# Optimization experiments

Measured on AMD Instinct MI355X. Metric: run time of the kernel, lower is better.

Reference implementation:

```python
import jax, jax.numpy as jnp
import numpy as np

G, NODES, H, E = 64, 511, 768, 4096
N = NODES + 1  # +1 graph token


def setup_inputs() -> dict:
    key = jax.random.key(0)
    ks = jax.random.split(key, 7)
    node_emb = jax.random.normal(ks[0], (4, H), dtype=jnp.float32) * 0.02
    node_emb = node_emb.at[0].set(0.0)  # padding_idx=0
    graph_emb = jax.random.normal(ks[1], (1, H), dtype=jnp.float32) * 0.02
    W_l = jax.random.normal(ks[2], (H, H), dtype=jnp.float32) / np.sqrt(H)
    b_l = jnp.zeros((H,), dtype=jnp.float32)
    W_r = jax.random.normal(ks[3], (H, H), dtype=jnp.float32) / np.sqrt(H)
    input_nodes = jax.random.randint(ks[4], (G, NODES), 0, 4, dtype=jnp.int64) if jax.config.jax_enable_x64 else jax.random.randint(ks[4], (G, NODES), 0, 4, dtype=jnp.int32)
    input_edges = jax.random.randint(ks[5], (G, 2, E), 0, N, dtype=jnp.int32)
    return {"input_nodes": input_nodes, "input_edges": input_edges,
            "node_emb": node_emb, "graph_emb": graph_emb,
            "W_l": W_l, "b_l": b_l, "W_r": W_r}


def _sage_conv(x, edges, W_l, b_l, W_r):
    # PyG SAGEConv (mean aggr): out = lin_l(mean_{j in N(i)} x_j) + lin_r(x_i)
    # x: [G, N, H]; edges: [G, 2, E] (row0 = src, row1 = dst)
    g, n, h = x.shape
    src, dst = edges[:, 0, :], edges[:, 1, :]                       # [G, E]
    offs = (jnp.arange(g, dtype=src.dtype) * n)[:, None]
    fs = (src + offs).reshape(-1)                                   # flat src ids
    fd = (dst + offs).reshape(-1)                                   # flat dst ids
    xf = x.reshape(g * n, h)
    msg = xf[fs]                                                    # gather [G*E, H]
    agg = jax.ops.segment_sum(msg, fd, num_segments=g * n)          # scatter-add
    deg = jax.ops.segment_sum(jnp.ones_like(fd, dtype=x.dtype), fd, num_segments=g * n)
    mean = agg / jnp.maximum(deg, 1.0)[:, None]
    out = mean @ W_l.T + b_l + xf @ W_r.T
    return out.reshape(g, n, h)


def reference(input_nodes, input_edges, node_emb, graph_emb, W_l, b_l, W_r):
    g = input_nodes.shape[0]
    node_feature = node_emb[input_nodes]                            # [G, NODES, H]
    graph_token = jnp.broadcast_to(graph_emb[None], (g, 1, node_emb.shape[1]))
    graph_node_feature = jnp.concatenate([graph_token, node_feature], axis=1)  # [G, N, H]
    graph_edge_feature = _sage_conv(graph_node_feature, input_edges, W_l, b_l, W_r)
    return (graph_node_feature, graph_edge_feature)
```

## Files before the change

kernel.cpp:

```cpp
#include <hip/hip_runtime.h>

#define G_     64
#define NODES_ 511
#define NN_    512
#define H_     768
#define E_     4096
#define NTYPE  5

typedef float f32x4 __attribute__((ext_vector_type(4)));

__global__ __launch_bounds__(512)
void prep_kernel(const int* __restrict__ edges,
                 const int* __restrict__ nodes,
                 const float* __restrict__ node_emb,
                 const float* __restrict__ graph_emb,
                 const float* __restrict__ W_l,
                 const float* __restrict__ b_l,
                 const float* __restrict__ W_r,
                 int* __restrict__ cnt,
                 float* __restrict__ P_l,
                 float* __restrict__ P_r)
{
    if (blockIdx.x < G_) {
        __shared__ int hist[NN_ * NTYPE];
        int g = blockIdx.x;
        int t = threadIdx.x;

        #pragma unroll
        for (int i = 0; i < NN_ * NTYPE / 512; ++i)
            hist[t + i * 512] = 0;
        __syncthreads();

        const int* eg = edges + (size_t)g * 2 * E_;
        const int* ng = nodes + (size_t)g * NODES_;
        #pragma unroll
        for (int i = 0; i < E_ / 512; ++i) {
            int e = t + i * 512;
            int src = eg[e];
            int dst = eg[E_ + e];
            int type = (src == 0) ? 0 : (ng[src - 1] + 1);
            atomicAdd(&hist[dst * NTYPE + type], 1);
        }
        __syncthreads();

        int* cg = cnt + (size_t)g * NN_ * NTYPE;
        #pragma unroll
        for (int i = 0; i < NN_ * NTYPE / 512; ++i)
            cg[t + i * 512] = hist[t + i * 512];
    } else {
        int wave = (blockIdx.x - G_) * 8 + (threadIdx.x >> 6);
        int lane = threadIdx.x & 63;
        int m = wave / (NTYPE * H_);
        int r = wave % (NTYPE * H_);
        int t = r / H_;
        int j = r % H_;
        const float* emb = (t == 0) ? graph_emb : (node_emb + (size_t)(t - 1) * H_);
        const float* W   = ((m == 0) ? W_l : W_r) + (size_t)j * H_;

        float a0, a1, a2;
        {
            int k0 = lane * 4;
            f32x4 w0 = *(const f32x4*)(W + k0);
            f32x4 e0 = *(const f32x4*)(emb + k0);
            f32x4 w1 = *(const f32x4*)(W + k0 + 256);
            f32x4 e1 = *(const f32x4*)(emb + k0 + 256);
            f32x4 w2 = *(const f32x4*)(W + k0 + 512);
            f32x4 e2 = *(const f32x4*)(emb + k0 + 512);
            a0 = w0.x * e0.x + w0.y * e0.y + w0.z * e0.z + w0.w * e0.w;
            a1 = w1.x * e1.x + w1.y * e1.y + w1.z * e1.z + w1.w * e1.w;
            a2 = w2.x * e2.x + w2.y * e2.y + w2.z * e2.z + w2.w * e2.w;
        }
        float acc = a0 + a1 + a2;
        #pragma unroll
        for (int off = 32; off; off >>= 1)
            acc += __shfl_xor(acc, off, 64);

        if (lane == 0) {
            if (m == 0) P_l[t * H_ + j] = acc;
            else        P_r[t * H_ + j] = acc + b_l[j];
        }
    }
}

__global__ __launch_bounds__(256)
void out_kernel(const int* __restrict__ nodes,
                const int* __restrict__ cnt,
                const float* __restrict__ node_emb,
                const float* __restrict__ graph_emb,
                const float* __restrict__ P_l,
                const float* __restrict__ P_r,
                float* __restrict__ gnf,
                float* __restrict__ gef)
{
    int wave = blockIdx.x * 4 + (threadIdx.x >> 6);
    int lane = threadIdx.x & 63;
    int k0   = lane * 4;

    f32x4 pl[NTYPE][3];
    #pragma unroll
    for (int t = 0; t < NTYPE; ++t) {
        #pragma unroll
        for (int c = 0; c < 3; ++c)
            pl[t][c] = *(const f32x4*)(P_l + (size_t)t * H_ + k0 + c * 256);
    }

    int row0 = wave * 4;
    #pragma unroll
    for (int i = 0; i < 4; ++i) {
        int row = row0 + i;
        int g = row >> 9;
        int n = row & (NN_ - 1);

        int ty = (n == 0) ? 0 : (nodes[g * NODES_ + n - 1] + 1);

        const int* c = cnt + (size_t)row * NTYPE;
        float c0 = (float)c[0], c1 = (float)c[1], c2 = (float)c[2],
              c3 = (float)c[3], c4 = (float)c[4];
        float inv = 1.0f / fmaxf(c0 + c1 + c2 + c3 + c4, 1.0f);
        float a0 = c0 * inv, a1 = c1 * inv, a2 = c2 * inv,
              a3 = c3 * inv, a4 = c4 * inv;

        const float* prr = P_r + (size_t)ty * H_;
        const float* er  = (ty == 0) ? graph_emb : (node_emb + (size_t)(ty - 1) * H_);
        size_t roff = (size_t)row * H_ + k0;

        #pragma unroll
        for (int ch = 0; ch < 3; ++ch) {
            f32x4 pr = *(const f32x4*)(prr + k0 + ch * 256);
            f32x4 ev = *(const f32x4*)(er  + k0 + ch * 256);
            f32x4 o  = a0 * pl[0][ch] + a1 * pl[1][ch] + a2 * pl[2][ch]
                     + a3 * pl[3][ch] + a4 * pl[4][ch] + pr;
            __builtin_nontemporal_store(ev, (f32x4*)(gnf + roff + ch * 256));
            __builtin_nontemporal_store(o,  (f32x4*)(gef + roff + ch * 256));
        }
    }
}

extern "C" void kernel_launch(void* const* d_in, const int* in_sizes, int n_in,
                              void* d_out, int out_size, void* d_ws, size_t ws_size,
                              hipStream_t stream)
{
    const int*   input_nodes = (const int*)d_in[0];
    const int*   input_edges = (const int*)d_in[1];
    const float* node_emb    = (const float*)d_in[2];
    const float* graph_emb   = (const float*)d_in[3];
    const float* W_l         = (const float*)d_in[4];
    const float* b_l         = (const float*)d_in[5];
    const float* W_r         = (const float*)d_in[6];

    float* gnf = (float*)d_out;
    float* gef = gnf + (size_t)G_ * NN_ * H_;

    int*   cnt = (int*)d_ws;
    size_t cnt_bytes = (size_t)G_ * NN_ * NTYPE * sizeof(int);
    float* P_l = (float*)((char*)d_ws + cnt_bytes);
    float* P_r = P_l + NTYPE * H_;

    prep_kernel<<<G_ + (2 * NTYPE * H_) / 8, 512, 0, stream>>>(
        input_edges, input_nodes, node_emb, graph_emb, W_l, b_l, W_r,
        cnt, P_l, P_r);

    out_kernel<<<(G_ * NN_) / 16, 256, 0, stream>>>(
        input_nodes, cnt, node_emb, graph_emb, P_l, P_r, gnf, gef);
}
```

Baseline: 228.9 us.

## Move gnf writes into prep kernel and precompute per-node mean coefficients

```diff
diff --git a/kernel.cpp b/kernel.cpp
--- a/kernel.cpp
+++ b/kernel.cpp
@@ -6,6 +6,9 @@
 #define H_     768
 #define E_     4096
 #define NTYPE  5
+
+#define PROJB_ 960
+#define GNFB_  2048
 
 typedef float f32x4 __attribute__((ext_vector_type(4)));
 
@@ -17,14 +20,15 @@
                  const float* __restrict__ W_l,
                  const float* __restrict__ b_l,
                  const float* __restrict__ W_r,
-                 int* __restrict__ cnt,
+                 float* __restrict__ params,
                  float* __restrict__ P_l,
-                 float* __restrict__ P_r)
+                 float* __restrict__ P_r,
+                 float* __restrict__ gnf)
 {
+    int t = threadIdx.x;
     if (blockIdx.x < G_) {
         __shared__ int hist[NN_ * NTYPE];
         int g = blockIdx.x;
-        int t = threadIdx.x;
 
         #pragma unroll
         for (int i = 0; i < NN_ * NTYPE / 512; ++i)
@@ -43,18 +47,29 @@
         }
         __syncthreads();
 
-        int* cg = cnt + (size_t)g * NN_ * NTYPE;
-        #pragma unroll
-        for (int i = 0; i < NN_ * NTYPE / 512; ++i)
-            cg[t + i * 512] = hist[t + i * 512];
-    } else {
-        int wave = (blockIdx.x - G_) * 8 + (threadIdx.x >> 6);
-        int lane = threadIdx.x & 63;
+        {
+            int n = t;
+            float c0 = (float)hist[n * NTYPE + 0];
+            float c1 = (float)hist[n * NTYPE + 1];
+            float c2 = (float)hist[n * NTYPE + 2];
+            float c3 = (float)hist[n * NTYPE + 3];
+            float c4 = (float)hist[n * NTYPE + 4];
+            float inv = 1.0f / fmaxf(c0 + c1 + c2 + c3 + c4, 1.0f);
+            int ty = (n == 0) ? 0 : (ng[n - 1] + 1);
+            f32x4 v0 = {c0 * inv, c1 * inv, c2 * inv, c3 * inv};
+            f32x4 v1 = {c4 * inv, __int_as_float(ty), 0.0f, 0.0f};
+            float* pp = params + ((size_t)g * NN_ + n) * 8;
+            *(f32x4*)pp       = v0;
+            *(f32x4*)(pp + 4) = v1;
+        }
+    } else if (blockIdx.x < G_ + PROJB_) {
+        int wave = (blockIdx.x - G_) * 8 + (t >> 6);
+        int lane = t & 63;
         int m = wave / (NTYPE * H_);
         int r = wave % (NTYPE * H_);
-        int t = r / H_;
+        int ty = r / H_;
         int j = r % H_;
-        const float* emb = (t == 0) ? graph_emb : (node_emb + (size_t)(t - 1) * H_);
+        const float* emb = (ty == 0) ? graph_emb : (node_emb + (size_t)(ty - 1) * H_);
         const float* W   = ((m == 0) ? W_l : W_r) + (size_t)j * H_;
 
         float a0, a1, a2;
@@ -76,20 +91,35 @@
             acc += __shfl_xor(acc, off, 64);
 
         if (lane == 0) {
-            if (m == 0) P_l[t * H_ + j] = acc;
-            else        P_r[t * H_ + j] = acc + b_l[j];
+            if (m == 0) P_l[ty * H_ + j] = acc;
+            else        P_r[ty * H_ + j] = acc + b_l[j];
+        }
+    } else {
+        int wv   = (blockIdx.x - (G_ + PROJB_)) * 8 + (t >> 6);
+        int lane = t & 63;
+        int k0   = lane * 4;
+        #pragma unroll
+        for (int i = 0; i < 2; ++i) {
+            int row = wv * 2 + i;
+            int g = row >> 9;
+            int n = row & (NN_ - 1);
+            int ty = (n == 0) ? 0 : (nodes[g * NODES_ + n - 1] + 1);
+            const float* er = (ty == 0) ? graph_emb
+                                        : (node_emb + (size_t)(ty - 1) * H_);
+            size_t roff = (size_t)row * H_ + k0;
+            #pragma unroll
+            for (int c = 0; c < 3; ++c) {
+                f32x4 ev = *(const f32x4*)(er + k0 + c * 256);
+                *(f32x4*)(gnf + roff + c * 256) = ev;
+            }
         }
     }
 }
 
 __global__ __launch_bounds__(256)
-void out_kernel(const int* __restrict__ nodes,
-                const int* __restrict__ cnt,
-                const float* __restrict__ node_emb,
-                const float* __restrict__ graph_emb,
+void gef_kernel(const float* __restrict__ params,
                 const float* __restrict__ P_l,
                 const float* __restrict__ P_r,
-                float* __restrict__ gnf,
                 float* __restrict__ gef)
 {
     int wave = blockIdx.x * 4 + (threadIdx.x >> 6);
@@ -98,40 +128,29 @@
 
     f32x4 pl[NTYPE][3];
     #pragma unroll
-    for (int t = 0; t < NTYPE; ++t) {
+    for (int tt = 0; tt < NTYPE; ++tt) {
         #pragma unroll
         for (int c = 0; c < 3; ++c)
-            pl[t][c] = *(const f32x4*)(P_l + (size_t)t * H_ + k0 + c * 256);
+            pl[tt][c] = *(const f32x4*)(P_l + (size_t)tt * H_ + k0 + c * 256);
     }
 
     int row0 = wave * 4;
     #pragma unroll
     for (int i = 0; i < 4; ++i) {
         int row = row0 + i;
-        int g = row >> 9;
-        int n = row & (NN_ - 1);
-
-        int ty = (n == 0) ? 0 : (nodes[g * NODES_ + n - 1] + 1);
-
-        const int* c = cnt + (size_t)row * NTYPE;
-        float c0 = (float)c[0], c1 = (float)c[1], c2 = (float)c[2],
-              c3 = (float)c[3], c4 = (float)c[4];
-        float inv = 1.0f / fmaxf(c0 + c1 + c2 + c3 + c4, 1.0f);
-        float a0 = c0 * inv, a1 = c1 * inv, a2 = c2 * inv,
-              a3 = c3 * inv, a4 = c4 * inv;
-
+        const float* pp = params + (size_t)row * 8;
+        f32x4 v0 = *(const f32x4*)pp;
+        f32x4 v1 = *(const f32x4*)(pp + 4);
+        int ty = __float_as_int(v1.y);
         const float* prr = P_r + (size_t)ty * H_;
-        const float* er  = (ty == 0) ? graph_emb : (node_emb + (size_t)(ty - 1) * H_);
         size_t roff = (size_t)row * H_ + k0;
 
         #pragma unroll
-        for (int ch = 0; ch < 3; ++ch) {
-            f32x4 pr = *(const f32x4*)(prr + k0 + ch * 256);
-            f32x4 ev = *(const f32x4*)(er  + k0 + ch * 256);
-            f32x4 o  = a0 * pl[0][ch] + a1 * pl[1][ch] + a2 * pl[2][ch]
-                     + a3 * pl[3][ch] + a4 * pl[4][ch] + pr;
-            __builtin_nontemporal_store(ev, (f32x4*)(gnf + roff + ch * 256));
-            __builtin_nontemporal_store(o,  (f32x4*)(gef + roff + ch * 256));
+        for (int c = 0; c < 3; ++c) {
+            f32x4 pr = *(const f32x4*)(prr + k0 + c * 256);
+            f32x4 o  = v0.x * pl[0][c] + v0.y * pl[1][c] + v0.z * pl[2][c]
+                     + v0.w * pl[3][c] + v1.x * pl[4][c] + pr;
+            *(f32x4*)(gef + roff + c * 256) = o;
         }
     }
 }
@@ -151,15 +170,14 @@
     float* gnf = (float*)d_out;
     float* gef = gnf + (size_t)G_ * NN_ * H_;
 
-    int*   cnt = (int*)d_ws;
-    size_t cnt_bytes = (size_t)G_ * NN_ * NTYPE * sizeof(int);
-    float* P_l = (float*)((char*)d_ws + cnt_bytes);
+    float* params = (float*)d_ws;
+    float* P_l = params + (size_t)G_ * NN_ * 8;
     float* P_r = P_l + NTYPE * H_;
 
-    prep_kernel<<<G_ + (2 * NTYPE * H_) / 8, 512, 0, stream>>>(
+    prep_kernel<<<G_ + PROJB_ + GNFB_, 512, 0, stream>>>(
         input_edges, input_nodes, node_emb, graph_emb, W_l, b_l, W_r,
-        cnt, P_l, P_r);
+        params, P_l, P_r, gnf);
 
-    out_kernel<<<(G_ * NN_) / 16, 256, 0, stream>>>(
-        input_nodes, cnt, node_emb, graph_emb, P_l, P_r, gnf, gef);
+    gef_kernel<<<(G_ * NN_) / 16, 256, 0, stream>>>(
+        params, P_l, P_r, gef);
 }
```

Result: faster. 215.1 us (-6.0%).
